# Performance work log

Hardware: AMD Instinct MI355X
Metric: run time of the kernel (lower is better)

## Reference

```python
import jax, jax.numpy as jnp
import numpy as np

N_NODES = 100000
N_EDGES = 500000
D = 256
EPS = 0.1  # GIN epsilon applied on self-loop relation


def setup_inputs() -> dict:
    key = jax.random.key(0)
    ks = jax.random.split(key, 9)
    return {
        "x": jax.random.normal(ks[0], (N_NODES, D), dtype=jnp.float32),
        "W_self": jax.random.normal(ks[1], (D, D), dtype=jnp.float32) * 0.05,
        "W_r1": jax.random.normal(ks[2], (D, D), dtype=jnp.float32) * 0.05,
        "W_r2": jax.random.normal(ks[3], (D, D), dtype=jnp.float32) * 0.05,
        "bias": jax.random.normal(ks[4], (D,), dtype=jnp.float32) * 0.05,
        "src1": jax.random.randint(ks[5], (N_EDGES,), 0, N_NODES, dtype=jnp.int32),
        "dst1": jax.random.randint(ks[6], (N_EDGES,), 0, N_NODES, dtype=jnp.int32),
        "src2": jax.random.randint(ks[7], (N_EDGES,), 0, N_NODES, dtype=jnp.int32),
        "dst2": jax.random.randint(ks[8], (N_EDGES,), 0, N_NODES, dtype=jnp.int32),
    }


def reference(x, W_self, W_r1, W_r2, bias, src1, dst1, src2, dst2):
    # self-loop relation: features scaled by (1+eps); one self-loop edge per node
    # so copy_u + sum delivers each node exactly its own message.
    h = (1.0 + EPS) * (x @ W_self)
    # regular relations: per-node message = x @ W, gathered along src edges,
    # scatter-summed at dst (DGL fn.copy_u + fn.sum, cross-etype 'sum' reducer).
    msg1 = x @ W_r1
    h = h + jax.ops.segment_sum(msg1[src1], dst1, num_segments=N_NODES)
    msg2 = x @ W_r2
    h = h + jax.ops.segment_sum(msg2[src2], dst2, num_segments=N_NODES)
    # bias + activation, then second activation (applied twice in original);
    # mlp/batch_norm are None, dropout is identity in eval.
    h = jax.nn.relu(h + bias)
    h = jax.nn.relu(h)
    return h
```

## Files before the change

kernel.cpp:

```cpp
#include <hip/hip_runtime.h>

#define N_NODES 100000
#define N_EDGES 500000
#define D 256
#define CAP 32
#define IDS_STRIDE 36
#define BM 64

typedef __bf16 bf16x8 __attribute__((ext_vector_type(8)));
typedef float  f32x4  __attribute__((ext_vector_type(4)));

__device__ __forceinline__ unsigned short f2bf(float f) {
    unsigned int u = __float_as_uint(f);
    u += 0x7fffu + ((u >> 16) & 1u);
    return (unsigned short)(u >> 16);
}
__device__ __forceinline__ float bfu_lo(unsigned u) { return __uint_as_float(u << 16); }
__device__ __forceinline__ float bfu_hi(unsigned u) { return __uint_as_float(u & 0xffff0000u); }

__device__ __forceinline__ void glds16(const unsigned short* g, unsigned short* l) {
    __builtin_amdgcn_global_load_lds(
        (const __attribute__((address_space(1))) unsigned int*)g,
        (__attribute__((address_space(3))) unsigned int*)l,
        16, 0, 0);
}

#define PREP_BLOCKS 17188

__global__ __launch_bounds__(256) void prep_kernel(
    const float* __restrict__ x, unsigned short* __restrict__ xb,
    const float* __restrict__ Ws, const float* __restrict__ W1,
    const float* __restrict__ W2, unsigned short* __restrict__ Wt,
    const int* __restrict__ src1, const int* __restrict__ dst1,
    const int* __restrict__ src2, const int* __restrict__ dst2,
    int* __restrict__ cnt1, int* __restrict__ cnt2,
    int* __restrict__ bkt1, int* __restrict__ bkt2)
{
    const int wid  = blockIdx.x * 4 + (threadIdx.x >> 6);
    const int lane = threadIdx.x & 63;
    const int group = wid / 22;
    const int pos   = wid - group * 22;

    if (pos < 16) {
        int cw = group * 16 + pos;
        if (cw >= 50000) return;
        size_t i = (size_t)cw * 512 + (size_t)lane * 8;
        float4 a = *(const float4*)(x + i);
        float4 c = *(const float4*)(x + i + 4);
        union { unsigned short s[8]; uint4 u; } o;
        o.s[0] = f2bf(a.x); o.s[1] = f2bf(a.y); o.s[2] = f2bf(a.z); o.s[3] = f2bf(a.w);
        o.s[4] = f2bf(c.x); o.s[5] = f2bf(c.y); o.s[6] = f2bf(c.z); o.s[7] = f2bf(c.w);
        *(uint4*)(xb + i) = o.u;
    } else if (pos < 21) {
        int bw = group * 5 + (pos - 16);
        int e = bw * 64 + lane;
        if (e >= 2 * N_EDGES) return;
        bool r2 = (e >= N_EDGES);
        const int* src = r2 ? src2 : src1;
        const int* dst = r2 ? dst2 : dst1;
        int* cnt = r2 ? cnt2 : cnt1;
        int* bkt = r2 ? bkt2 : bkt1;
        int ei = r2 ? e - N_EDGES : e;
        int s = src[ei], d = dst[ei];
        int p = atomicAdd(&cnt[d], 1);
        if (p < CAP) bkt[d * CAP + p] = s;
    } else {
        int idx = group * 64 + lane;
        if (idx >= 3 * D * D) return;
        int k = idx >> 8;
        int n = idx & (D - 1);
        const float* W = (k < D) ? Ws : (k < 2 * D ? W1 : W2);
        float scale = (k < D) ? 1.1f : 1.0f;
        int dk = k ^ ((((n >> 1) & 3)) << 3);
        Wt[(size_t)n * (3 * D) + dk] = f2bf(W[(size_t)(k & (D - 1)) * D + n] * scale);
    }
}

__global__ __launch_bounds__(512, 4) void gemm_kernel(
    const unsigned short* __restrict__ xb,
    const int* __restrict__ cnt1, const int* __restrict__ cnt2,
    const int* __restrict__ bkt1, const int* __restrict__ bkt2,
    const unsigned short* __restrict__ Wt,
    const float* __restrict__ bias, float* __restrict__ out)
{
    __shared__ unsigned short Alds[2][BM * 32];
    __shared__ unsigned short Blds[2][256 * 32];
    __shared__ int idsL[2 * BM * IDS_STRIDE];

    const int tid  = threadIdx.x;
    const int lane = tid & 63;
    const int wave = tid >> 6;
    const int quad = lane >> 4;
    const int l15  = lane & 15;
    const int m0 = blockIdx.x * BM;
    const int wm = (wave >> 2) * 32;
    const int wn = (wave & 3) * 64;

    const int rowA = tid >> 3;
    const int tg   = tid & 7;
    int mA = m0 + rowA; if (mA >= N_NODES) mA = N_NODES - 1;
    const int wAoff = rowA * 32 + (((tg & 3) ^ ((rowA >> 1) & 3)) * 8);
    const int swz = (l15 >> 1) & 3;

    const int gr   = lane >> 2;
    const int gch  = lane & 3;
    const int gswz = (lane >> 3) & 3;
    int mSelf = m0 + (wave << 4) + gr;
    if (mSelf >= N_NODES) mSelf = N_NODES - 1;
    const unsigned short* aSelfSrc = xb + (size_t)mSelf * D + ((gch ^ gswz) << 3);
    const unsigned short* bSrc0 = Wt + (size_t)((wave << 4) + gr) * (3 * D) + (gch << 3);
    const unsigned short* bSrc1 = bSrc0 + (size_t)128 * (3 * D);

    {
        int rel = tid >> 8;
        int idx = tid & 255;
        int n   = idx >> 2;
        int h   = (idx & 3) << 3;
        int nc  = m0 + n; if (nc >= N_NODES) nc = N_NODES - 1;
        const int* bsrc = (rel ? bkt2 : bkt1) + (size_t)nc * CAP + h;
        int* ldst = idsL + (rel * BM + n) * IDS_STRIDE + h;
        uint4 q0 = *(const uint4*)(bsrc + 0);
        uint4 q1 = *(const uint4*)(bsrc + 4);
        *(uint4*)(ldst + 0) = q0;
        *(uint4*)(ldst + 4) = q1;
    }

    int c1 = cnt1[mA]; if (c1 > CAP) c1 = CAP;
    int c2 = cnt2[mA]; if (c2 > CAP) c2 = CAP;

    if (wave < 4) glds16(aSelfSrc, &Alds[0][wave * 512]);
    glds16(bSrc0, &Blds[0][wave * 512]);
    glds16(bSrc1, &Blds[0][4096 + wave * 512]);

    f32x4 acc[2][4] = {};
    uint4 gv0[4];
    uint4 ra;
    int cc = 0;
    const int* myids = idsL;
    const unsigned short* gbase = xb;

    __syncthreads();

    #define FOLD(v) { s0 += bfu_lo((v).x); s1 += bfu_hi((v).x); \
                      s2 += bfu_lo((v).y); s3 += bfu_hi((v).y); \
                      s4 += bfu_lo((v).z); s5 += bfu_hi((v).z); \
                      s6 += bfu_lo((v).w); s7 += bfu_hi((v).w); }

    for (int kt = 0; kt < 24; ++kt) {
        const int cur = kt & 1, nxt = cur ^ 1;
        const int ktn = kt + 1;
        const bool odd = kt & 1;
        const bool oddWork = odd && kt >= 7 && kt <= 21;

        if (ktn < 24) {
            if (ktn < 8) { if (wave < 4) glds16(aSelfSrc + ktn * 32, &Alds[nxt][wave * 512]); }
            glds16(bSrc0 + ktn * 32, &Blds[nxt][wave * 512]);
            glds16(bSrc1 + ktn * 32, &Blds[nxt][4096 + wave * 512]);
        }

        float s0 = 0.f, s1 = 0.f, s2 = 0.f, s3 = 0.f,
              s4 = 0.f, s5 = 0.f, s6 = 0.f, s7 = 0.f;
        uint4 gv1[6];

        if (!odd) {
            if (kt >= 8 && tg >= 4)
                *(uint4*)(&Alds[nxt][wAoff]) = ra;
            if (kt >= 6 && kt <= 20) {
                const int S = kt + 2;
                const bool r2g = (S >= 16);
                cc    = r2g ? c2 : c1;
                myids = idsL + ((r2g ? BM : 0) + rowA) * IDS_STRIDE;
                gbase = xb + ((S - 8) & 7) * 32 + tg * 8;
                #pragma unroll
                for (int e = 0; e < 4; ++e)
                    if (e < cc) gv0[e] = *(const uint4*)(gbase + (size_t)myids[e] * D);
            }
        } else if (oddWork) {
            #pragma unroll
            for (int e = 4; e < 10; ++e)
                if (e < cc) gv1[e - 4] = *(const uint4*)(gbase + (size_t)myids[e] * D);
            #pragma unroll
            for (int e = 0; e < 4; ++e)
                if (e < cc) FOLD(gv0[e]);
        }

        {
            const unsigned short* Ab = Alds[cur];
            const unsigned short* Bb = Blds[cur];
            bf16x8 b0f = *(const bf16x8*)(Bb + (wn +  0 + l15) * 32 + ((quad ^ swz) * 8));
            bf16x8 b1f = *(const bf16x8*)(Bb + (wn + 16 + l15) * 32 + ((quad ^ swz) * 8));
            bf16x8 b2f = *(const bf16x8*)(Bb + (wn + 32 + l15) * 32 + ((quad ^ swz) * 8));
            bf16x8 b3f = *(const bf16x8*)(Bb + (wn + 48 + l15) * 32 + ((quad ^ swz) * 8));
            #pragma unroll
            for (int i = 0; i < 2; ++i) {
                bf16x8 afi = *(const bf16x8*)(Ab + (wm + i * 16 + l15) * 32 + ((quad ^ swz) * 8));
                acc[i][0] = __builtin_amdgcn_mfma_f32_16x16x32_bf16(afi, b0f, acc[i][0], 0, 0, 0);
                acc[i][1] = __builtin_amdgcn_mfma_f32_16x16x32_bf16(afi, b1f, acc[i][1], 0, 0, 0);
                acc[i][2] = __builtin_amdgcn_mfma_f32_16x16x32_bf16(afi, b2f, acc[i][2], 0, 0, 0);
                acc[i][3] = __builtin_amdgcn_mfma_f32_16x16x32_bf16(afi, b3f, acc[i][3], 0, 0, 0);
            }
        }

        if (oddWork) {
            #pragma unroll
            for (int e = 4; e < 10; ++e)
                if (e < cc) FOLD(gv1[e - 4]);
            for (int e = 10; e < cc; ++e) {
                uint4 t = *(const uint4*)(gbase + (size_t)myids[e] * D);
                FOLD(t);
            }
            ra.x = (unsigned)f2bf(s0) | ((unsigned)f2bf(s1) << 16);
            ra.y = (unsigned)f2bf(s2) | ((unsigned)f2bf(s3) << 16);
            ra.z = (unsigned)f2bf(s4) | ((unsigned)f2bf(s5) << 16);
            ra.w = (unsigned)f2bf(s6) | ((unsigned)f2bf(s7) << 16);
            if (tg < 4)
                *(uint4*)(&Alds[nxt][wAoff]) = ra;
        }
        __syncthreads();
    }
    #undef FOLD

    #pragma unroll
    for (int j = 0; j < 4; ++j) {
        int col = wn + j * 16 + l15;
        float bj = bias[col];
        #pragma unroll
        for (int i = 0; i < 2; ++i) {
            int rb = m0 + wm + i * 16 + quad * 4;
            #pragma unroll
            for (int r = 0; r < 4; ++r) {
                int m = rb + r;
                if (m < N_NODES)
                    __builtin_nontemporal_store(
                        fmaxf(acc[i][j][r] + bj, 0.f),
                        out + (size_t)m * D + col);
            }
        }
    }
}

extern "C" void kernel_launch(void* const* d_in, const int* in_sizes, int n_in,
                              void* d_out, int out_size, void* d_ws, size_t ws_size,
                              hipStream_t stream) {
    const float* x    = (const float*)d_in[0];
    const float* Ws   = (const float*)d_in[1];
    const float* W1   = (const float*)d_in[2];
    const float* W2   = (const float*)d_in[3];
    const float* bias = (const float*)d_in[4];
    const int* src1   = (const int*)d_in[5];
    const int* dst1   = (const int*)d_in[6];
    const int* src2   = (const int*)d_in[7];
    const int* dst2   = (const int*)d_in[8];
    float* out = (float*)d_out;

    char* p = (char*)d_ws;
    unsigned short* xb  = (unsigned short*)p; p += (size_t)N_NODES * D * 2;
    int* cnt1 = (int*)p; p += (size_t)N_NODES * 4;
    int* cnt2 = (int*)p; p += (size_t)N_NODES * 4;
    int* bkt1 = (int*)p; p += (size_t)N_NODES * CAP * 4;
    int* bkt2 = (int*)p; p += (size_t)N_NODES * CAP * 4;
    unsigned short* Wt = (unsigned short*)p;

    (void)hipMemsetAsync(cnt1, 0, (size_t)2 * N_NODES * 4, stream);

    prep_kernel<<<PREP_BLOCKS, 256, 0, stream>>>(
        x, xb, Ws, W1, W2, Wt, src1, dst1, src2, dst2, cnt1, cnt2, bkt1, bkt2);

    gemm_kernel<<<(N_NODES + BM - 1) / BM, 512, 0, stream>>>(
        xb, cnt1, cnt2, bkt1, bkt2, Wt, bias, out);
}
```

Measured before the change: 416.0 us.

## Replace software-pipelined per-K-slice gather with full-row wave gather into LDS

Drops the interleaved schedule where each K-slice of neighbor rows was gathered and folded between MFMA steps. Each wave now gathers whole 256-wide neighbor rows for 8 nodes, using lane-shuffled source ids and 8-byte loads per lane, and writes the full aggregated A tile for one relation into a larger swizzled LDS buffer. The GEMM then runs over it in three phases (self, rel1, rel2) with sync barriers between them. This gives fully coalesced 512-byte row reads instead of 64-byte slice reads, but loses the overlap of gather latency with MFMA work and uses more LDS, which may reduce occupancy. The x-to-bf16 prep store pattern is also changed to 4-element chunks.

```diff
diff --git a/kernel.cpp b/kernel.cpp
--- a/kernel.cpp
+++ b/kernel.cpp
@@ -4,8 +4,8 @@
 #define N_EDGES 500000
 #define D 256
 #define CAP 32
-#define IDS_STRIDE 36
 #define BM 64
+#define AG_STRIDE 2056
 
 typedef __bf16 bf16x8 __attribute__((ext_vector_type(8)));
 typedef float  f32x4  __attribute__((ext_vector_type(4)));
@@ -15,8 +15,9 @@
     u += 0x7fffu + ((u >> 16) & 1u);
     return (unsigned short)(u >> 16);
 }
-__device__ __forceinline__ float bfu_lo(unsigned u) { return __uint_as_float(u << 16); }
-__device__ __forceinline__ float bfu_hi(unsigned u) { return __uint_as_float(u & 0xffff0000u); }
+__device__ __forceinline__ float bf2f(unsigned short b) {
+    return __uint_as_float(((unsigned int)b) << 16);
+}
 
 __device__ __forceinline__ void glds16(const unsigned short* g, unsigned short* l) {
     __builtin_amdgcn_global_load_lds(
@@ -44,13 +45,14 @@
     if (pos < 16) {
         int cw = group * 16 + pos;
         if (cw >= 50000) return;
-        size_t i = (size_t)cw * 512 + (size_t)lane * 8;
-        float4 a = *(const float4*)(x + i);
-        float4 c = *(const float4*)(x + i + 4);
-        union { unsigned short s[8]; uint4 u; } o;
-        o.s[0] = f2bf(a.x); o.s[1] = f2bf(a.y); o.s[2] = f2bf(a.z); o.s[3] = f2bf(a.w);
-        o.s[4] = f2bf(c.x); o.s[5] = f2bf(c.y); o.s[6] = f2bf(c.z); o.s[7] = f2bf(c.w);
-        *(uint4*)(xb + i) = o.u;
+        size_t base = (size_t)cw * 512;
+        float4 a = *(const float4*)(x + base + lane * 4);
+        float4 c = *(const float4*)(x + base + 256 + lane * 4);
+        ushort4 oa, oc;
+        oa.x = f2bf(a.x); oa.y = f2bf(a.y); oa.z = f2bf(a.z); oa.w = f2bf(a.w);
+        oc.x = f2bf(c.x); oc.y = f2bf(c.y); oc.z = f2bf(c.z); oc.w = f2bf(c.w);
+        *(ushort4*)(xb + base + lane * 4) = oa;
+        *(ushort4*)(xb + base + 256 + lane * 4) = oc;
     } else if (pos < 21) {
         int bw = group * 5 + (pos - 16);
         int e = bw * 64 + lane;
@@ -83,9 +85,9 @@
     const unsigned short* __restrict__ Wt,
     const float* __restrict__ bias, float* __restrict__ out)
 {
-    __shared__ unsigned short Alds[2][BM * 32];
+    __shared__ unsigned short Agth[8 * AG_STRIDE];
+    __shared__ unsigned short Aslf[2][BM * 32];
     __shared__ unsigned short Blds[2][256 * 32];
-    __shared__ int idsL[2 * BM * IDS_STRIDE];
 
     const int tid  = threadIdx.x;
     const int lane = tid & 63;
@@ -95,11 +97,6 @@
     const int m0 = blockIdx.x * BM;
     const int wm = (wave >> 2) * 32;
     const int wn = (wave & 3) * 64;
-
-    const int rowA = tid >> 3;
-    const int tg   = tid & 7;
-    int mA = m0 + rowA; if (mA >= N_NODES) mA = N_NODES - 1;
-    const int wAoff = rowA * 32 + (((tg & 3) ^ ((rowA >> 1) & 3)) * 8);
     const int swz = (l15 >> 1) & 3;
 
     const int gr   = lane >> 2;
@@ -111,114 +108,86 @@
     const unsigned short* bSrc0 = Wt + (size_t)((wave << 4) + gr) * (3 * D) + (gch << 3);
     const unsigned short* bSrc1 = bSrc0 + (size_t)128 * (3 * D);
 
-    {
-        int rel = tid >> 8;
-        int idx = tid & 255;
-        int n   = idx >> 2;
-        int h   = (idx & 3) << 3;
-        int nc  = m0 + n; if (nc >= N_NODES) nc = N_NODES - 1;
-        const int* bsrc = (rel ? bkt2 : bkt1) + (size_t)nc * CAP + h;
-        int* ldst = idsL + (rel * BM + n) * IDS_STRIDE + h;
-        uint4 q0 = *(const uint4*)(bsrc + 0);
-        uint4 q1 = *(const uint4*)(bsrc + 4);
-        *(uint4*)(ldst + 0) = q0;
-        *(uint4*)(ldst + 4) = q1;
-    }
-
-    int c1 = cnt1[mA]; if (c1 > CAP) c1 = CAP;
-    int c2 = cnt2[mA]; if (c2 > CAP) c2 = CAP;
-
-    if (wave < 4) glds16(aSelfSrc, &Alds[0][wave * 512]);
+    auto gather_rel = [&](const int* __restrict__ cnt, const int* __restrict__ bkt) {
+        #pragma unroll 1
+        for (int i = 0; i < 8; ++i) {
+            const int n = (wave << 3) + i;
+            int g = m0 + n; if (g >= N_NODES) g = N_NODES - 1;
+            int c = cnt[g]; if (c > CAP) c = CAP;
+            int sid = (lane < c) ? bkt[(size_t)g * CAP + lane] : 0;
+            float a0 = 0.f, a1 = 0.f, a2 = 0.f, a3 = 0.f;
+            ushort4 v[8];
+            #pragma unroll
+            for (int t = 0; t < 8; ++t)
+                if (t < c) v[t] = *(const ushort4*)(xb + (size_t)__shfl(sid, t) * D + lane * 4);
+            #pragma unroll
+            for (int t = 0; t < 8; ++t)
+                if (t < c) {
+                    a0 += bf2f(v[t].x); a1 += bf2f(v[t].y);
+                    a2 += bf2f(v[t].z); a3 += bf2f(v[t].w);
+                }
+            for (int e = 8; e < c; ++e) {
+                ushort4 tv = *(const ushort4*)(xb + (size_t)__shfl(sid, e) * D + lane * 4);
+                a0 += bf2f(tv.x); a1 += bf2f(tv.y); a2 += bf2f(tv.z); a3 += bf2f(tv.w);
+            }
+            ushort4 o;
+            o.x = f2bf(a0); o.y = f2bf(a1); o.z = f2bf(a2); o.w = f2bf(a3);
+            const int tq = lane >> 3;
+            const int qp = ((lane >> 1) & 3) ^ ((n >> 1) & 3);
+            *(ushort4*)(Agth + tq * AG_STRIDE + n * 32 + qp * 8 + (lane & 1) * 4) = o;
+        }
+    };
+
+    f32x4 acc[2][4] = {};
+    auto mfma_tile = [&](const unsigned short* Ab, const unsigned short* Bb) {
+        bf16x8 b0f = *(const bf16x8*)(Bb + (wn +  0 + l15) * 32 + ((quad ^ swz) * 8));
+        bf16x8 b1f = *(const bf16x8*)(Bb + (wn + 16 + l15) * 32 + ((quad ^ swz) * 8));
+        bf16x8 b2f = *(const bf16x8*)(Bb + (wn + 32 + l15) * 32 + ((quad ^ swz) * 8));
+        bf16x8 b3f = *(const bf16x8*)(Bb + (wn + 48 + l15) * 32 + ((quad ^ swz) * 8));
+        #pragma unroll
+        for (int i = 0; i < 2; ++i) {
+            bf16x8 afi = *(const bf16x8*)(Ab + (wm + i * 16 + l15) * 32 + ((quad ^ swz) * 8));
+            acc[i][0] = __builtin_amdgcn_mfma_f32_16x16x32_bf16(afi, b0f, acc[i][0], 0, 0, 0);
+            acc[i][1] = __builtin_amdgcn_mfma_f32_16x16x32_bf16(afi, b1f, acc[i][1], 0, 0, 0);
+            acc[i][2] = __builtin_amdgcn_mfma_f32_16x16x32_bf16(afi, b2f, acc[i][2], 0, 0, 0);
+            acc[i][3] = __builtin_amdgcn_mfma_f32_16x16x32_bf16(afi, b3f, acc[i][3], 0, 0, 0);
+        }
+    };
+
+    if (wave < 4) glds16(aSelfSrc, &Aslf[0][wave * 512]);
     glds16(bSrc0, &Blds[0][wave * 512]);
     glds16(bSrc1, &Blds[0][4096 + wave * 512]);
 
-    f32x4 acc[2][4] = {};
-    uint4 gv0[4];
-    uint4 ra;
-    int cc = 0;
-    const int* myids = idsL;
-    const unsigned short* gbase = xb;
-
+    gather_rel(cnt1, bkt1);
     __syncthreads();
 
-    #define FOLD(v) { s0 += bfu_lo((v).x); s1 += bfu_hi((v).x); \
-                      s2 += bfu_lo((v).y); s3 += bfu_hi((v).y); \
-                      s4 += bfu_lo((v).z); s5 += bfu_hi((v).z); \
-                      s6 += bfu_lo((v).w); s7 += bfu_hi((v).w); }
-
-    for (int kt = 0; kt < 24; ++kt) {
-        const int cur = kt & 1, nxt = cur ^ 1;
+    for (int kt = 0; kt < 16; ++kt) {
         const int ktn = kt + 1;
-        const bool odd = kt & 1;
-        const bool oddWork = odd && kt >= 7 && kt <= 21;
-
+        if (ktn < 8 && wave < 4)
+            glds16(aSelfSrc + ktn * 32, &Aslf[ktn & 1][wave * 512]);
+        if (ktn < 16) {
+            glds16(bSrc0 + ktn * 32, &Blds[ktn & 1][wave * 512]);
+            glds16(bSrc1 + ktn * 32, &Blds[ktn & 1][4096 + wave * 512]);
+        }
+        const unsigned short* Ab = (kt < 8) ? &Aslf[kt & 1][0] : (Agth + (kt - 8) * AG_STRIDE);
+        mfma_tile(Ab, &Blds[kt & 1][0]);
+        __syncthreads();
+    }
+
+    glds16(bSrc0 + 16 * 32, &Blds[0][wave * 512]);
+    glds16(bSrc1 + 16 * 32, &Blds[0][4096 + wave * 512]);
+    gather_rel(cnt2, bkt2);
+    __syncthreads();
+
+    for (int kt = 16; kt < 24; ++kt) {
+        const int ktn = kt + 1;
         if (ktn < 24) {
-            if (ktn < 8) { if (wave < 4) glds16(aSelfSrc + ktn * 32, &Alds[nxt][wave * 512]); }
-            glds16(bSrc0 + ktn * 32, &Blds[nxt][wave * 512]);
-            glds16(bSrc1 + ktn * 32, &Blds[nxt][4096 + wave * 512]);
-        }
-
-        float s0 = 0.f, s1 = 0.f, s2 = 0.f, s3 = 0.f,
-              s4 = 0.f, s5 = 0.f, s6 = 0.f, s7 = 0.f;
-        uint4 gv1[6];
-
-        if (!odd) {
-            if (kt >= 8 && tg >= 4)
-                *(uint4*)(&Alds[nxt][wAoff]) = ra;
-            if (kt >= 6 && kt <= 20) {
-                const int S = kt + 2;
-                const bool r2g = (S >= 16);
-                cc    = r2g ? c2 : c1;
-                myids = idsL + ((r2g ? BM : 0) + rowA) * IDS_STRIDE;
-                gbase = xb + ((S - 8) & 7) * 32 + tg * 8;
-                #pragma unroll
-                for (int e = 0; e < 4; ++e)
-                    if (e < cc) gv0[e] = *(const uint4*)(gbase + (size_t)myids[e] * D);
-            }
-        } else if (oddWork) {
-            #pragma unroll
-            for (int e = 4; e < 10; ++e)
-                if (e < cc) gv1[e - 4] = *(const uint4*)(gbase + (size_t)myids[e] * D);
-            #pragma unroll
-            for (int e = 0; e < 4; ++e)
-                if (e < cc) FOLD(gv0[e]);
-        }
-
-        {
-            const unsigned short* Ab = Alds[cur];
-            const unsigned short* Bb = Blds[cur];
-            bf16x8 b0f = *(const bf16x8*)(Bb + (wn +  0 + l15) * 32 + ((quad ^ swz) * 8));
-            bf16x8 b1f = *(const bf16x8*)(Bb + (wn + 16 + l15) * 32 + ((quad ^ swz) * 8));
-            bf16x8 b2f = *(const bf16x8*)(Bb + (wn + 32 + l15) * 32 + ((quad ^ swz) * 8));
-            bf16x8 b3f = *(const bf16x8*)(Bb + (wn + 48 + l15) * 32 + ((quad ^ swz) * 8));
-            #pragma unroll
-            for (int i = 0; i < 2; ++i) {
-                bf16x8 afi = *(const bf16x8*)(Ab + (wm + i * 16 + l15) * 32 + ((quad ^ swz) * 8));
-                acc[i][0] = __builtin_amdgcn_mfma_f32_16x16x32_bf16(afi, b0f, acc[i][0], 0, 0, 0);
-                acc[i][1] = __builtin_amdgcn_mfma_f32_16x16x32_bf16(afi, b1f, acc[i][1], 0, 0, 0);
-                acc[i][2] = __builtin_amdgcn_mfma_f32_16x16x32_bf16(afi, b2f, acc[i][2], 0, 0, 0);
-                acc[i][3] = __builtin_amdgcn_mfma_f32_16x16x32_bf16(afi, b3f, acc[i][3], 0, 0, 0);
-            }
-        }
-
-        if (oddWork) {
-            #pragma unroll
-            for (int e = 4; e < 10; ++e)
-                if (e < cc) FOLD(gv1[e - 4]);
-            for (int e = 10; e < cc; ++e) {
-                uint4 t = *(const uint4*)(gbase + (size_t)myids[e] * D);
-                FOLD(t);
-            }
-            ra.x = (unsigned)f2bf(s0) | ((unsigned)f2bf(s1) << 16);
-            ra.y = (unsigned)f2bf(s2) | ((unsigned)f2bf(s3) << 16);
-            ra.z = (unsigned)f2bf(s4) | ((unsigned)f2bf(s5) << 16);
-            ra.w = (unsigned)f2bf(s6) | ((unsigned)f2bf(s7) << 16);
-            if (tg < 4)
-                *(uint4*)(&Alds[nxt][wAoff]) = ra;
-        }
+            glds16(bSrc0 + ktn * 32, &Blds[ktn & 1][wave * 512]);
+            glds16(bSrc1 + ktn * 32, &Blds[ktn & 1][4096 + wave * 512]);
+        }
+        mfma_tile(Agth + (kt - 16) * AG_STRIDE, &Blds[kt & 1][0]);
         __syncthreads();
     }
-    #undef FOLD
 
     #pragma unroll
     for (int j = 0; j < 4; ++j) {
```

After: 481.0 us. +15.6%, slower.
